# Kernel tuning notes

Hardware: AMD Instinct MI355X
Metric: run time of the kernel (lower is better)

## Reference

```python
import jax, jax.numpy as jnp
import numpy as np

N_BINS = 10  # rho thresholds 0.1..0.9 -> bin ids 0..9

def setup_inputs() -> dict:
    key = jax.random.key(0)
    k1, k2, k3 = jax.random.split(key, 3)
    B, D, G = 4_000_000, 11, 10
    z_1 = jax.random.uniform(k1, (B, D), dtype=jnp.float32)
    z_2 = jax.random.uniform(k2, (B, D), dtype=jnp.float32)
    dist_grade = jax.random.uniform(k3, (B, G), dtype=jnp.float32)
    return {"z_1": z_1, "z_2": z_2, "dist_grade": dist_grade}

def reference(z_1, z_2, dist_grade):
    # to_center: (x1, x2) columns -> center coords proxy, shape [2, B]
    dx = z_2[:, 0] - z_1[:, 0]
    dy = -(z_2[:, 2] - z_1[:, 2])  # dir_vec[1] = -dir_vec[1]
    rho = jnp.sqrt(dx * dx + dy * dy)  # [B]
    # threshold binning: dist_id = #{k in 1..9 : rho >= k/10}
    thresholds = jnp.arange(1, N_BINS, dtype=jnp.float32) * 0.1  # [9]
    dist_id = jnp.sum(rho[:, None] >= thresholds[None, :], axis=-1).astype(jnp.int32)  # [B]
    # one-hot scatter then weighted sum == gather along bins
    out = jnp.take_along_axis(dist_grade, dist_id[:, None], axis=1)[:, 0]  # [B]
    return out
```

## Files before the change

### kernel.cpp

```cpp
#include <hip/hip_runtime.h>


#define ZD 11
#define GD 10

__global__ __launch_bounds__(256) void rho_valuation_kernel(
    const float* __restrict__ z1,
    const float* __restrict__ z2,
    const float* __restrict__ dg,
    float* __restrict__ out,
    int B)
{
    int b = blockIdx.x * blockDim.x + threadIdx.x;
    if (b >= B) return;

    long off = (long)b * ZD;
    float a0 = z1[off + 0];
    float a2 = z1[off + 2];
    float c0 = z2[off + 0];
    float c2 = z2[off + 2];

    float dx = __fadd_rn(c0, -a0);
    float dy = __fadd_rn(a2, -c2);

    float s   = __fadd_rn(__fmul_rn(dx, dx), __fmul_rn(dy, dy));
    float rho = __fsqrt_rn(s);

    int id = 0;
    #pragma unroll
    for (int k = 1; k <= 9; ++k) {
        id += (rho >= (float)k * 0.1f) ? 1 : 0;
    }

    out[b] = dg[(long)b * GD + id];
}

extern "C" void kernel_launch(void* const* d_in, const int* in_sizes, int n_in,
                              void* d_out, int out_size, void* d_ws, size_t ws_size,
                              hipStream_t stream) {
    const float* z1 = (const float*)d_in[0];
    const float* z2 = (const float*)d_in[1];
    const float* dg = (const float*)d_in[2];
    float* out = (float*)d_out;

    int B = out_size;
    const int block = 256;
    int grid = (B + block - 1) / block;
    rho_valuation_kernel<<<grid, block, 0, stream>>>(z1, z2, dg, out, B);
}
```

Measured before the change: 436.1 us.

## Stage row tiles into shared memory with coalesced float4 loads

Each block now copies its 256-row tiles of z_1, z_2 and dist_grade into LDS using coalesced float4 loads, then computes rho and does the gather from shared memory. This replaces the strided per-thread scalar global loads, which touch rows 44 or 40 bytes apart. It also loads full rows, including the 7 unused columns of z_1 and z_2. The cost is about 32 KB of LDS per block, which may limit occupancy, plus an extra barrier. A scalar fallback path handles the tail block.

Result: no change. 431.1 us (-1.1%).

```diff
diff --git a/kernel.cpp b/kernel.cpp
--- a/kernel.cpp
+++ b/kernel.cpp
@@ -3,6 +3,7 @@
 
 #define ZD 11
 #define GD 10
+#define ROWS 256
 
 __global__ __launch_bounds__(256) void rho_valuation_kernel(
     const float* __restrict__ z1,
@@ -11,28 +12,67 @@
     float* __restrict__ out,
     int B)
 {
-    int b = blockIdx.x * blockDim.x + threadIdx.x;
-    if (b >= B) return;
+    __shared__ float s_z1[ROWS * ZD];
+    __shared__ float s_z2[ROWS * ZD];
+    __shared__ float s_dg[ROWS * GD];
 
-    long off = (long)b * ZD;
-    float a0 = z1[off + 0];
-    float a2 = z1[off + 2];
-    float c0 = z2[off + 0];
-    float c2 = z2[off + 2];
+    const int t = threadIdx.x;
+    const long base = (long)blockIdx.x * ROWS;
 
-    float dx = __fadd_rn(c0, -a0);
-    float dy = __fadd_rn(a2, -c2);
+    if (base + ROWS <= B) {
+        const float4* g1 = (const float4*)(z1 + base * ZD);
+        const float4* g2 = (const float4*)(z2 + base * ZD);
+        const float4* g3 = (const float4*)(dg + base * GD);
+        float4* l1 = (float4*)s_z1;
+        float4* l2 = (float4*)s_z2;
+        float4* l3 = (float4*)s_dg;
 
-    float s   = __fadd_rn(__fmul_rn(dx, dx), __fmul_rn(dy, dy));
-    float rho = __fsqrt_rn(s);
+        #pragma unroll
+        for (int i = 0; i < 3; ++i) {
+            int idx = t + i * 256;
+            if (idx < (ROWS * ZD) / 4) { l1[idx] = g1[idx]; l2[idx] = g2[idx]; }
+        }
+        #pragma unroll
+        for (int i = 0; i < 3; ++i) {
+            int idx = t + i * 256;
+            if (idx < (ROWS * GD) / 4) { l3[idx] = g3[idx]; }
+        }
+        __syncthreads();
 
-    int id = 0;
-    #pragma unroll
-    for (int k = 1; k <= 9; ++k) {
-        id += (rho >= (float)k * 0.1f) ? 1 : 0;
+        float a0 = s_z1[t * ZD + 0];
+        float a2 = s_z1[t * ZD + 2];
+        float c0 = s_z2[t * ZD + 0];
+        float c2 = s_z2[t * ZD + 2];
+
+        float dx = __fadd_rn(c0, -a0);
+        float dy = __fadd_rn(a2, -c2);
+        float s   = __fadd_rn(__fmul_rn(dx, dx), __fmul_rn(dy, dy));
+        float rho = __fsqrt_rn(s);
+
+        int id = 0;
+        #pragma unroll
+        for (int k = 1; k <= 9; ++k)
+            id += (rho >= (float)k * 0.1f) ? 1 : 0;
+
+        out[base + t] = s_dg[t * GD + id];
+    } else {
+        long b = base + t;
+        if (b < B) {
+            float a0 = z1[b * ZD + 0];
+            float a2 = z1[b * ZD + 2];
+            float c0 = z2[b * ZD + 0];
+            float c2 = z2[b * ZD + 2];
+            float dx = __fadd_rn(c0, -a0);
+            float dy = __fadd_rn(a2, -c2);
+            float s   = __fadd_rn(__fmul_rn(dx, dx), __fmul_rn(dy, dy));
+            float rho = __fsqrt_rn(s);
+            int id = 0;
+            #pragma unroll
+            for (int k = 1; k <= 9; ++k)
+                id += (rho >= (float)k * 0.1f) ? 1 : 0;
+            out[b] = dg[b * GD + id];
+        }
     }
-
-    out[b] = dg[(long)b * GD + id];
 }
 
 extern "C" void kernel_launch(void* const* d_in, const int* in_sizes, int n_in,
@@ -44,7 +84,7 @@
     float* out = (float*)d_out;
 
     int B = out_size;
-    const int block = 256;
+    const int block = ROWS;
     int grid = (B + block - 1) / block;
     rho_valuation_kernel<<<grid, block, 0, stream>>>(z1, z2, dg, out, B);
 }
```
